# Optimization experiments

Measured on AMD Instinct MI355X. Metric: run time of the kernel, lower is better.

The kernel has to match this reference:

```python
import jax, jax.numpy as jnp
import numpy as np

N, NS, CIN, COUT, S = 65536, 16, 64, 64, 8
MID = COUT  # mid_planes = out_planes // 1
EPS = 1e-5


def _bn(t, g, b):
    # BatchNorm1d in training mode: normalize per channel over (points, neighbors)
    m = jnp.mean(t, axis=(0, 1), keepdims=True)
    v = jnp.var(t, axis=(0, 1), keepdims=True)
    return (t - m) * jax.lax.rsqrt(v + EPS) * g + b


def setup_inputs() -> dict:
    key = jax.random.key(0)
    ks = jax.random.split(key, 16)

    def w(k, shape, fan_in):
        return (jax.random.normal(k, shape, jnp.float32) / np.sqrt(fan_in)).astype(jnp.float32)

    return {
        "p": jax.random.uniform(ks[0], (N, 3), jnp.float32),
        "x": jax.random.normal(ks[1], (N, CIN), jnp.float32),
        "idx": jax.random.randint(ks[2], (N, NS), 0, N, jnp.int32),
        # q/k/v linears
        "Wq": w(ks[3], (CIN, MID), CIN), "bq": jnp.zeros((MID,), jnp.float32),
        "Wk": w(ks[4], (CIN, MID), CIN), "bk": jnp.zeros((MID,), jnp.float32),
        "Wv": w(ks[5], (CIN, COUT), CIN), "bv": jnp.zeros((COUT,), jnp.float32),
        # linear_p: Linear(3,3) -> BN(3) -> ReLU -> Linear(3,out)
        "Wp1": w(ks[6], (3, 3), 3), "bp1": jnp.zeros((3,), jnp.float32),
        "gp": jnp.ones((3,), jnp.float32), "bp_bn": jnp.zeros((3,), jnp.float32),
        "Wp2": w(ks[7], (3, COUT), 3), "bp2": jnp.zeros((COUT,), jnp.float32),
        # linear_w: BN(mid)->ReLU->Linear(mid,mid//s)->BN->ReLU->Linear(mid//s,mid//s)
        "gw1": jnp.ones((MID,), jnp.float32), "bw1_bn": jnp.zeros((MID,), jnp.float32),
        "Ww1": w(ks[8], (MID, MID // S), MID), "bw1": jnp.zeros((MID // S,), jnp.float32),
        "gw2": jnp.ones((MID // S,), jnp.float32), "bw2_bn": jnp.zeros((MID // S,), jnp.float32),
        "Ww2": w(ks[9], (MID // S, MID // S), MID // S), "bw2": jnp.zeros((MID // S,), jnp.float32),
    }


def reference(p, x, idx, Wq, bq, Wk, bk, Wv, bv, Wp1, bp1, gp, bp_bn, Wp2, bp2,
              gw1, bw1_bn, Ww1, bw1, gw2, bw2_bn, Ww2, bw2):
    # per-point projections
    xq = x @ Wq + bq                       # [N, MID]
    xk = x @ Wk + bk                       # [N, MID]
    xv = x @ Wv + bv                       # [N, COUT]
    # queryandgroup: gather neighbor features + relative xyz
    rel_p = p[idx] - p[:, None, :]         # [N, NS, 3]
    xk_g = xk[idx]                         # [N, NS, MID]
    xv_g = xv[idx]                         # [N, NS, COUT]
    # linear_p MLP on relative positions
    pr = rel_p @ Wp1 + bp1
    pr = jax.nn.relu(_bn(pr, gp, bp_bn))
    pr = pr @ Wp2 + bp2                    # [N, NS, COUT]
    # subtractive attention logits (out//mid == 1, so p_r sum is identity)
    w = xk_g - xq[:, None, :] + pr         # [N, NS, MID]
    # linear_w MLP
    w = jax.nn.relu(_bn(w, gw1, bw1_bn))
    w = w @ Ww1 + bw1                      # [N, NS, MID//S]
    w = jax.nn.relu(_bn(w, gw2, bw2_bn))
    w = w @ Ww2 + bw2                      # [N, NS, COUT//S]
    w = jax.nn.softmax(w, axis=1)          # softmax over neighbors
    # grouped weighted aggregation with shared attention planes
    n, ns, c = xv_g.shape
    out = ((xv_g + pr).reshape(n, ns, S, c // S) * w[:, :, None, :]).sum(1)
    return out.reshape(n, c)
```

## Files before the change

kernel.cpp:

```cpp
#include <hip/hip_runtime.h>

typedef unsigned short u16;
typedef __attribute__((ext_vector_type(8))) short bf16x8;
typedef __attribute__((ext_vector_type(8))) unsigned short u16x8;
typedef __attribute__((ext_vector_type(4))) float f32x4;

#define NPTS 65536
#define MTOT 1048576
#define M2TOT 131072
#define EPSb 1e-5f

#define XQ_OFF  0u
#define T_OFF   4194304u
#define ST_OFF  15728640u
#define XK_US   31457792u
#define XV_US   35652096u
#define WTQ_US  14680064u
#define WT1_US  14692352u

__device__ __forceinline__ float bf2f(u16 h) {
    return __uint_as_float(((unsigned)h) << 16);
}
__device__ __forceinline__ u16 f2bf(float f) {
    unsigned u = __float_as_uint(f);
    u += 0x7fffu + ((u >> 16) & 1u);
    return (u16)(u >> 16);
}
__device__ __forceinline__ u16 f2bf_fast(float f) {
    return (u16)((__float_as_uint(f) + 0x8000u) >> 16);
}

__global__ __launch_bounds__(256) void k0_prep(
    const float* __restrict__ Wq, const float* __restrict__ Wk,
    const float* __restrict__ Wv, const float* __restrict__ Ww1,
    float* __restrict__ ws)
{
    u16* wsu = (u16*)ws;
    const int gid = blockIdx.x * 256 + threadIdx.x;
    if (gid < 12288) {
        const float* W = (gid < 4096) ? Wq : ((gid < 8192) ? Wk : Wv);
        const int rem = gid & 4095;
        const int n = rem >> 6, c = rem & 63;
        wsu[WTQ_US + (unsigned)gid] = f2bf(W[c * 64 + n]);
    } else if (gid < 12800) {
        const int rem = gid - 12288;
        const int c = rem >> 6, r = rem & 63;
        wsu[WT1_US + (unsigned)rem] = f2bf(Ww1[r * 8 + c]);
    }
}

__global__ __launch_bounds__(256) void k1_proj_bn1(
    const float* __restrict__ p, const float* __restrict__ x, const int* __restrict__ idx,
    const float* __restrict__ bq, const float* __restrict__ bk, const float* __restrict__ bv,
    const float* __restrict__ Wp1, const float* __restrict__ bp1,
    float* __restrict__ ws)
{
    u16* wsu = (u16*)ws;
    __shared__ float sred[6];
    const int tid   = threadIdx.x;
    const int lane  = tid & 63;
    const int wid   = tid >> 6;
    const int col16 = lane & 15;
    const int quad  = lane >> 4;
    if (tid < 6) sred[tid] = 0.0f;
    __syncthreads();

    bf16x8 bf[3][4][2];
#pragma unroll
    for (int M = 0; M < 3; ++M)
#pragma unroll
        for (int t = 0; t < 4; ++t)
#pragma unroll
            for (int h = 0; h < 2; ++h)
                bf[M][t][h] = *(const bf16x8*)&wsu[WTQ_US +
                    (unsigned)(M * 4096 + (t * 16 + col16) * 64 + h * 32 + quad * 8)];

    float bq_t[4], bk_t[4], bv_t[4];
#pragma unroll
    for (int t = 0; t < 4; ++t) {
        bq_t[t] = bq[t * 16 + col16];
        bk_t[t] = bk[t * 16 + col16];
        bv_t[t] = bv[t * 16 + col16];
    }

    float* xq   = ws + XQ_OFF;
    u16*  xkb   = wsu + XK_US;
    u16*  xvb   = wsu + XV_US;

    const int gw = blockIdx.x * 4 + wid;
#pragma unroll
    for (int g = 0; g < 2; ++g) {
        const int n0 = (gw * 2 + g) * 16;
        const float* xrow = x + (unsigned)(n0 + col16) * 64u;
        const float4 fa0 = *(const float4*)&xrow[quad * 8];
        const float4 fa1 = *(const float4*)&xrow[quad * 8 + 4];
        const float4 fb0 = *(const float4*)&xrow[32 + quad * 8];
        const float4 fb1 = *(const float4*)&xrow[32 + quad * 8 + 4];
        bf16x8 a0, a1;
        a0[0] = (short)f2bf_fast(fa0.x); a0[1] = (short)f2bf_fast(fa0.y);
        a0[2] = (short)f2bf_fast(fa0.z); a0[3] = (short)f2bf_fast(fa0.w);
        a0[4] = (short)f2bf_fast(fa1.x); a0[5] = (short)f2bf_fast(fa1.y);
        a0[6] = (short)f2bf_fast(fa1.z); a0[7] = (short)f2bf_fast(fa1.w);
        a1[0] = (short)f2bf_fast(fb0.x); a1[1] = (short)f2bf_fast(fb0.y);
        a1[2] = (short)f2bf_fast(fb0.z); a1[3] = (short)f2bf_fast(fb0.w);
        a1[4] = (short)f2bf_fast(fb1.x); a1[5] = (short)f2bf_fast(fb1.y);
        a1[6] = (short)f2bf_fast(fb1.z); a1[7] = (short)f2bf_fast(fb1.w);

#pragma unroll
        for (int t = 0; t < 4; ++t) {
            f32x4 aq = {0,0,0,0}, ak = {0,0,0,0}, av = {0,0,0,0};
            aq = __builtin_amdgcn_mfma_f32_16x16x32_bf16(a0, bf[0][t][0], aq, 0, 0, 0);
            aq = __builtin_amdgcn_mfma_f32_16x16x32_bf16(a1, bf[0][t][1], aq, 0, 0, 0);
            ak = __builtin_amdgcn_mfma_f32_16x16x32_bf16(a0, bf[1][t][0], ak, 0, 0, 0);
            ak = __builtin_amdgcn_mfma_f32_16x16x32_bf16(a1, bf[1][t][1], ak, 0, 0, 0);
            av = __builtin_amdgcn_mfma_f32_16x16x32_bf16(a0, bf[2][t][0], av, 0, 0, 0);
            av = __builtin_amdgcn_mfma_f32_16x16x32_bf16(a1, bf[2][t][1], av, 0, 0, 0);
#pragma unroll
            for (int r = 0; r < 4; ++r) {
                const unsigned row = (unsigned)(n0 + quad * 4 + r);
                const unsigned o   = row * 64u + (unsigned)(t * 16 + col16);
                xq[o]  = aq[r] + bq_t[t];
                xkb[o] = f2bf(ak[r] + bk_t[t]);
                xvb[o] = f2bf(av[r] + bv_t[t]);
            }
        }
    }

    const int base = blockIdx.x * 128;
    const float w00 = Wp1[0], w01 = Wp1[1], w02 = Wp1[2];
    const float w10 = Wp1[3], w11 = Wp1[4], w12 = Wp1[5];
    const float w20 = Wp1[6], w21 = Wp1[7], w22 = Wp1[8];
    const float c0 = bp1[0], c1 = bp1[1], c2 = bp1[2];
    float s0 = 0, s1 = 0, s2 = 0, q0 = 0, q1 = 0, q2 = 0;
#pragma unroll
    for (int m = 0; m < 8; ++m) {
        const int pl = tid + m * 256;
        const int n  = base + (pl >> 4);
        const unsigned gpair = (unsigned)(base * 16 + pl);
        const int nb = idx[gpair];
        const float r0 = p[nb * 3 + 0] - p[n * 3 + 0];
        const float r1 = p[nb * 3 + 1] - p[n * 3 + 1];
        const float r2 = p[nb * 3 + 2] - p[n * 3 + 2];
        const float t0 = c0 + r0 * w00 + r1 * w10 + r2 * w20;
        const float t1 = c1 + r0 * w01 + r1 * w11 + r2 * w21;
        const float t2 = c2 + r0 * w02 + r1 * w12 + r2 * w22;
        ws[T_OFF + gpair * 3u + 0u] = t0;
        ws[T_OFF + gpair * 3u + 1u] = t1;
        ws[T_OFF + gpair * 3u + 2u] = t2;
        s0 += t0; s1 += t1; s2 += t2;
        q0 += t0 * t0; q1 += t1 * t1; q2 += t2 * t2;
    }
    atomicAdd(&sred[0], s0); atomicAdd(&sred[1], s1); atomicAdd(&sred[2], s2);
    atomicAdd(&sred[3], q0); atomicAdd(&sred[4], q1); atomicAdd(&sred[5], q2);
    __syncthreads();
    if (tid < 6) atomicAdd(&ws[ST_OFF + tid], sred[tid]);
}

__global__ __launch_bounds__(256) void k1b_bn1apply(
    const float* __restrict__ gp, const float* __restrict__ bp_bn,
    float* __restrict__ ws)
{
    const float invM = 1.0f / (float)MTOT;
    float A1[3], B1[3];
#pragma unroll
    for (int a = 0; a < 3; ++a) {
        const float mean = ws[ST_OFF + a] * invM;
        const float var  = ws[ST_OFF + 3 + a] * invM - mean * mean;
        const float sc = gp[a] * rsqrtf(var + EPSb);
        A1[a] = sc; B1[a] = bp_bn[a] - mean * sc;
    }
    const unsigned t = blockIdx.x * 256u + threadIdx.x;
    float4* Tp = (float4*)(ws + T_OFF + t * 12u);
    float4 v0 = Tp[0], v1 = Tp[1], v2 = Tp[2];
    v0.x = fmaxf(fmaf(v0.x, A1[0], B1[0]), 0.0f);
    v0.y = fmaxf(fmaf(v0.y, A1[1], B1[1]), 0.0f);
    v0.z = fmaxf(fmaf(v0.z, A1[2], B1[2]), 0.0f);
    v0.w = fmaxf(fmaf(v0.w, A1[0], B1[0]), 0.0f);
    v1.x = fmaxf(fmaf(v1.x, A1[1], B1[1]), 0.0f);
    v1.y = fmaxf(fmaf(v1.y, A1[2], B1[2]), 0.0f);
    v1.z = fmaxf(fmaf(v1.z, A1[0], B1[0]), 0.0f);
    v1.w = fmaxf(fmaf(v1.w, A1[1], B1[1]), 0.0f);
    v2.x = fmaxf(fmaf(v2.x, A1[2], B1[2]), 0.0f);
    v2.y = fmaxf(fmaf(v2.y, A1[0], B1[0]), 0.0f);
    v2.z = fmaxf(fmaf(v2.z, A1[1], B1[1]), 0.0f);
    v2.w = fmaxf(fmaf(v2.w, A1[2], B1[2]), 0.0f);
    Tp[0] = v0; Tp[1] = v1; Tp[2] = v2;
}

__global__ __launch_bounds__(256) void k2_bn2(
    const int* __restrict__ idx,
    const float* __restrict__ Wp2, const float* __restrict__ bp2,
    float* __restrict__ ws)
{
    u16* wsu = (u16*)ws;
    __shared__ float ss[64], sq[64];
    const int tid = threadIdx.x;
    const int lane = tid & 63;
    const int gw = blockIdx.x * 4 + (tid >> 6);
    if (tid < 64) { ss[tid] = 0.0f; sq[tid] = 0.0f; }

    const float wp20 = Wp2[lane], wp21 = Wp2[64 + lane], wp22 = Wp2[128 + lane];
    const float bp2c = bp2[lane];
    const float* xq  = ws + XQ_OFF;
    const float* T   = ws + T_OFF;
    const u16*  xkb  = wsu + XK_US;

    float s = 0.0f, q = 0.0f;

    for (int nn = 0; nn < 4; ++nn) {
        const int nu = __builtin_amdgcn_readfirstlane((gw * 4 + nn) * 8);

        const int4* ir4 = (const int4*)(idx + (unsigned)nu * 16u);
        const int4 i0 = ir4[0], i1 = ir4[1], i2 = ir4[2], i3 = ir4[3];
        const int nbs[16] = { i0.x, i0.y, i0.z, i0.w, i1.x, i1.y, i1.z, i1.w,
                              i2.x, i2.y, i2.z, i2.w, i3.x, i3.y, i3.z, i3.w };
        u16 kr[16];
#pragma unroll
        for (int j = 0; j < 16; ++j) kr[j] = xkb[(unsigned)nbs[j] * 64u + lane];

        float tr[48];
        const float4* Tr4 = (const float4*)(T + (unsigned)nu * 48u);
#pragma unroll
        for (int c = 0; c < 12; ++c) {
            const float4 v = Tr4[c];
            tr[4 * c + 0] = v.x; tr[4 * c + 1] = v.y;
            tr[4 * c + 2] = v.z; tr[4 * c + 3] = v.w;
        }
        const float xqc  = xq[(unsigned)nu * 64u + lane];
        const float base = bp2c - xqc;

#pragma unroll
        for (int j = 0; j < 16; ++j) {
            const float prx = base + tr[3 * j + 0] * wp20
                                   + tr[3 * j + 1] * wp21
                                   + tr[3 * j + 2] * wp22;
            const float w0 = bf2f(kr[j]) + prx;
            s += w0; q = fmaf(w0, w0, q);
        }
    }
    __syncthreads();
    atomicAdd(&ss[lane], s); atomicAdd(&sq[lane], q);
    __syncthreads();
    if (tid < 64) {
        atomicAdd(&ws[ST_OFF + 6 + tid], ss[tid]);
        atomicAdd(&ws[ST_OFF + 70 + tid], sq[tid]);
    }
}

__global__ __launch_bounds__(256) void k2b_bn3(
    const int* __restrict__ idx,
    const float* __restrict__ Wp2, const float* __restrict__ bp2,
    const float* __restrict__ gw1, const float* __restrict__ bw1_bn,
    const float* __restrict__ bw1,
    float* __restrict__ ws)
{
    u16* wsu = (u16*)ws;
    __shared__ float s3r[8], q3r[8];
    const int tid   = threadIdx.x;
    const int lane  = tid & 63;
    const int wid   = tid >> 6;
    const int col16 = lane & 15;
    const int quad  = lane >> 4;
    if (tid < 8) { s3r[tid] = 0.0f; q3r[tid] = 0.0f; }
    __syncthreads();

    const float invM2 = 1.0f / (float)M2TOT;
    float A2A[8], DA[8], WA0[8], WA1[8], WA2[8];
    float A2B[8], DB[8], WB0[8], WB1[8], WB2[8];
#pragma unroll
    for (int i = 0; i < 8; ++i) {
        {
            const int k = quad * 8 + i;
            const float mean = ws[ST_OFF + 6 + k] * invM2;
            const float var  = ws[ST_OFF + 70 + k] * invM2 - mean * mean;
            const float A2 = gw1[k] * rsqrtf(var + EPSb);
            const float B2 = bw1_bn[k] - mean * A2;
            A2A[i] = A2;
            DA[i]  = fmaf(A2, bp2[k], B2);
            WA0[i] = A2 * Wp2[k]; WA1[i] = A2 * Wp2[64 + k]; WA2[i] = A2 * Wp2[128 + k];
        }
        {
            const int k = 32 + quad * 8 + i;
            const float mean = ws[ST_OFF + 6 + k] * invM2;
            const float var  = ws[ST_OFF + 70 + k] * invM2 - mean * mean;
            const float A2 = gw1[k] * rsqrtf(var + EPSb);
            const float B2 = bw1_bn[k] - mean * A2;
            A2B[i] = A2;
            DB[i]  = fmaf(A2, bp2[k], B2);
            WB0[i] = A2 * Wp2[k]; WB1[i] = A2 * Wp2[64 + k]; WB2[i] = A2 * Wp2[128 + k];
        }
    }
    bf16x8 b0 = {0,0,0,0,0,0,0,0}, b1 = {0,0,0,0,0,0,0,0};
    if (col16 < 8) {
        b0 = *(const bf16x8*)&wsu[WT1_US + (unsigned)(col16 * 64 + quad * 8)];
        b1 = *(const bf16x8*)&wsu[WT1_US + (unsigned)(col16 * 64 + 32 + quad * 8)];
    }
    const float bw1c = (col16 < 8) ? bw1[col16] : 0.0f;

    const float* xq  = ws + XQ_OFF;
    const float* T   = ws + T_OFF;
    const u16*  xkb  = wsu + XK_US;
    const int sg = (blockIdx.x * 4 + wid) * 8;
    float bs = 0.0f, bq2 = 0.0f;

    for (int it = 0; it < 8; ++it) {
        const int nu = __builtin_amdgcn_readfirstlane((sg + it) * 8);

        const int nbv = idx[(unsigned)nu * 16u + (unsigned)col16];
        const u16* grow = xkb + (unsigned)nbv * 64u;
        const u16x8 gA = *(const u16x8*)(grow + quad * 8);
        const u16x8 gB = *(const u16x8*)(grow + 32 + quad * 8);

        const float* Trow = T + (unsigned)nu * 48u + (unsigned)col16 * 3u;
        float t0 = Trow[0];
        float t1 = Trow[1];
        float t2 = Trow[2];

        const float* xr = xq + (unsigned)nu * 64u;
        const float4 x0 = *(const float4*)(xr + quad * 8);
        const float4 x1 = *(const float4*)(xr + quad * 8 + 4);
        const float4 x2 = *(const float4*)(xr + 32 + quad * 8);
        const float4 x3 = *(const float4*)(xr + 32 + quad * 8 + 4);
        const float xqA[8] = { x0.x, x0.y, x0.z, x0.w, x1.x, x1.y, x1.z, x1.w };
        const float xqB[8] = { x2.x, x2.y, x2.z, x2.w, x3.x, x3.y, x3.z, x3.w };

        bf16x8 a0, a1;
#pragma unroll
        for (int i = 0; i < 8; ++i) {
            float vA = fmaf(-A2A[i], xqA[i], DA[i]);
            vA = fmaf(t0, WA0[i], vA);
            vA = fmaf(t1, WA1[i], vA);
            vA = fmaf(t2, WA2[i], vA);
            vA = fmaf(A2A[i], bf2f(gA[i]), vA);
            a0[i] = (short)f2bf_fast(fmaxf(vA, 0.0f));

            float vB = fmaf(-A2B[i], xqB[i], DB[i]);
            vB = fmaf(t0, WB0[i], vB);
            vB = fmaf(t1, WB1[i], vB);
            vB = fmaf(t2, WB2[i], vB);
            vB = fmaf(A2B[i], bf2f(gB[i]), vB);
            a1[i] = (short)f2bf_fast(fmaxf(vB, 0.0f));
        }
        f32x4 acc = {0.0f, 0.0f, 0.0f, 0.0f};
        acc = __builtin_amdgcn_mfma_f32_16x16x32_bf16(a0, b0, acc, 0, 0, 0);
        acc = __builtin_amdgcn_mfma_f32_16x16x32_bf16(a1, b1, acc, 0, 0, 0);
        if (col16 < 8) {
#pragma unroll
            for (int r = 0; r < 4; ++r) {
                const float o = acc[r] + bw1c;
                bs += o;
                bq2 = fmaf(o, o, bq2);
            }
        }
    }
    if (col16 < 8) {
        atomicAdd(&s3r[col16], bs);
        atomicAdd(&q3r[col16], bq2);
    }
    __syncthreads();
    if (tid < 8) {
        atomicAdd(&ws[ST_OFF + 134 + tid], s3r[tid]);
        atomicAdd(&ws[ST_OFF + 142 + tid], q3r[tid]);
    }
}

__global__ __launch_bounds__(256) void k34_fused(
    const int* __restrict__ idx,
    const float* __restrict__ Wp2, const float* __restrict__ bp2,
    const float* __restrict__ gw1, const float* __restrict__ bw1_bn,
    const float* __restrict__ bw1,
    const float* __restrict__ gw2, const float* __restrict__ bw2_bn,
    const float* __restrict__ Ww2, const float* __restrict__ bw2,
    const float* __restrict__ ws, float* __restrict__ out)
{
    const u16* wsu = (const u16*)ws;
    __shared__ float sv3[4][16][8];
    __shared__ float se[4][16][8];
    const int tid   = threadIdx.x;
    const int lane  = tid & 63;
    const int wid   = tid >> 6;
    const int col16 = lane & 15;
    const int quad  = lane >> 4;
    const int tt    = lane & 7;
    const int j1    = lane >> 3;

    const float invM2 = 1.0f / (float)M2TOT;
    float A2A[8], DA[8], WA0[8], WA1[8], WA2[8];
    float A2B[8], DB[8], WB0[8], WB1[8], WB2[8];
#pragma unroll
    for (int i = 0; i < 8; ++i) {
        {
            const int k = quad * 8 + i;
            const float mean = ws[ST_OFF + 6 + k] * invM2;
            const float var  = ws[ST_OFF + 70 + k] * invM2 - mean * mean;
            const float A2 = gw1[k] * rsqrtf(var + EPSb);
            const float B2 = bw1_bn[k] - mean * A2;
            A2A[i] = A2;
            DA[i]  = fmaf(A2, bp2[k], B2);
            WA0[i] = A2 * Wp2[k]; WA1[i] = A2 * Wp2[64 + k]; WA2[i] = A2 * Wp2[128 + k];
        }
        {
            const int k = 32 + quad * 8 + i;
            const float mean = ws[ST_OFF + 6 + k] * invM2;
            const float var  = ws[ST_OFF + 70 + k] * invM2 - mean * mean;
            const float A2 = gw1[k] * rsqrtf(var + EPSb);
            const float B2 = bw1_bn[k] - mean * A2;
            A2B[i] = A2;
            DB[i]  = fmaf(A2, bp2[k], B2);
            WB0[i] = A2 * Wp2[k]; WB1[i] = A2 * Wp2[64 + k]; WB2[i] = A2 * Wp2[128 + k];
        }
    }
    bf16x8 b0 = {0,0,0,0,0,0,0,0}, b1 = {0,0,0,0,0,0,0,0};
    if (col16 < 8) {
        b0 = *(const bf16x8*)&wsu[WT1_US + (unsigned)(col16 * 64 + quad * 8)];
        b1 = *(const bf16x8*)&wsu[WT1_US + (unsigned)(col16 * 64 + 32 + quad * 8)];
    }
    const float bw1c = (col16 < 8) ? bw1[col16] : 0.0f;
    const int   c3    = col16 & 7;
    const float mean3 = ws[ST_OFF + 134 + c3] * invM2;
    const float var3  = ws[ST_OFF + 142 + c3] * invM2 - mean3 * mean3;
    const float A3c   = gw2[c3] * rsqrtf(var3 + EPSb);
    const float B3f   = fmaf(A3c, bw1c, bw2_bn[c3] - mean3 * A3c);
    float ww2c[8];
#pragma unroll
    for (int u = 0; u < 8; ++u) ww2c[u] = Ww2[u * 8 + tt];
    const float bw2c = bw2[tt];
    const float wp20 = Wp2[lane], wp21 = Wp2[64 + lane], wp22 = Wp2[128 + lane];
    const float bp2c = bp2[lane];

    const float* xq  = ws + XQ_OFF;
    const float* T   = ws + T_OFF;
    const u16*  xkb  = wsu + XK_US;
    const u16*  xvb  = wsu + XV_US;

    const int n0 = (blockIdx.x * 4 + wid) * 16;
    for (int it = 0; it < 16; ++it) {
        const int nu = __builtin_amdgcn_readfirstlane(n0 + it);

        const int4* ir4 = (const int4*)(idx + (unsigned)nu * 16u);
        const int4 i0 = ir4[0], i1 = ir4[1], i2 = ir4[2], i3 = ir4[3];
        const int nbs[16] = { i0.x, i0.y, i0.z, i0.w, i1.x, i1.y, i1.z, i1.w,
                              i2.x, i2.y, i2.z, i2.w, i3.x, i3.y, i3.z, i3.w };
        const int nbv = idx[(unsigned)nu * 16u + (unsigned)col16];
        const u16* grow = xkb + (unsigned)nbv * 64u;
        const u16x8 gA = *(const u16x8*)(grow + quad * 8);
        const u16x8 gB = *(const u16x8*)(grow + 32 + quad * 8);
        u16 xvr[16];
#pragma unroll
        for (int j = 0; j < 16; ++j) xvr[j] = xvb[(unsigned)nbs[j] * 64u + lane];

        const float* Trow = T + (unsigned)nu * 48u + (unsigned)col16 * 3u;
        const float t0 = Trow[0];
        const float t1 = Trow[1];
        const float t2 = Trow[2];
        float tr[48];
        const float4* Tr4 = (const float4*)(T + (unsigned)nu * 48u);
#pragma unroll
        for (int c = 0; c < 12; ++c) {
            const float4 v = Tr4[c];
            tr[4 * c + 0] = v.x; tr[4 * c + 1] = v.y;
            tr[4 * c + 2] = v.z; tr[4 * c + 3] = v.w;
        }
        const float* xr = xq + (unsigned)nu * 64u;
        const float4 x0 = *(const float4*)(xr + quad * 8);
        const float4 x1 = *(const float4*)(xr + quad * 8 + 4);
        const float4 x2 = *(const float4*)(xr + 32 + quad * 8);
        const float4 x3 = *(const float4*)(xr + 32 + quad * 8 + 4);
        const float xqA[8] = { x0.x, x0.y, x0.z, x0.w, x1.x, x1.y, x1.z, x1.w };
        const float xqB[8] = { x2.x, x2.y, x2.z, x2.w, x3.x, x3.y, x3.z, x3.w };

        bf16x8 a0, a1;
#pragma unroll
        for (int i = 0; i < 8; ++i) {
            float vA = fmaf(-A2A[i], xqA[i], DA[i]);
            vA = fmaf(t0, WA0[i], vA);
            vA = fmaf(t1, WA1[i], vA);
            vA = fmaf(t2, WA2[i], vA);
            vA = fmaf(A2A[i], bf2f(gA[i]), vA);
            a0[i] = (short)f2bf_fast(fmaxf(vA, 0.0f));

            float vB = fmaf(-A2B[i], xqB[i], DB[i]);
            vB = fmaf(t0, WB0[i], vB);
            vB = fmaf(t1, WB1[i], vB);
            vB = fmaf(t2, WB2[i], vB);
            vB = fmaf(A2B[i], bf2f(gB[i]), vB);
            a1[i] = (short)f2bf_fast(fmaxf(vB, 0.0f));
        }
        f32x4 acc = {0.0f, 0.0f, 0.0f, 0.0f};
        acc = __builtin_amdgcn_mfma_f32_16x16x32_bf16(a0, b0, acc, 0, 0, 0);
        acc = __builtin_amdgcn_mfma_f32_16x16x32_bf16(a1, b1, acc, 0, 0, 0);

        if (col16 < 8) {
#pragma unroll
            for (int r = 0; r < 4; ++r)
                sv3[wid][quad * 4 + r][col16] = fmaxf(fmaf(A3c, acc[r], B3f), 0.0f);
        }
        float s0 = bw2c, s1 = bw2c;
#pragma unroll
        for (int u = 0; u < 8; ++u) {
            s0 = fmaf(sv3[wid][j1][u], ww2c[u], s0);
            s1 = fmaf(sv3[wid][j1 + 8][u], ww2c[u], s1);
        }
        float mx = fmaxf(s0, s1);
        mx = fmaxf(mx, __shfl_xor(mx, 8));
        mx = fmaxf(mx, __shfl_xor(mx, 16));
        mx = fmaxf(mx, __shfl_xor(mx, 32));
        const float e0 = __expf(s0 - mx);
        const float e1 = __expf(s1 - mx);
        float sm = e0 + e1;
        sm += __shfl_xor(sm, 8);
        sm += __shfl_xor(sm, 16);
        sm += __shfl_xor(sm, 32);
        const float rs = __builtin_amdgcn_rcpf(sm);
        se[wid][j1][tt]     = e0 * rs;
        se[wid][j1 + 8][tt] = e1 * rs;

        float xvacc = 0.0f, ta0 = 0.0f, ta1 = 0.0f, ta2 = 0.0f;
#pragma unroll
        for (int j = 0; j < 16; ++j) {
            const float ej = se[wid][j][tt];
            xvacc = fmaf(bf2f(xvr[j]), ej, xvacc);
            ta0 = fmaf(tr[3 * j + 0], ej, ta0);
            ta1 = fmaf(tr[3 * j + 1], ej, ta1);
            ta2 = fmaf(tr[3 * j + 2], ej, ta2);
        }
        out[(unsigned)nu * 64u + lane] =
            fmaf(ta0, wp20, fmaf(ta1, wp21, fmaf(ta2, wp22, xvacc + bp2c)));
    }
}

extern "C" void kernel_launch(void* const* d_in, const int* in_sizes, int n_in,
                              void* d_out, int out_size, void* d_ws, size_t ws_size,
                              hipStream_t stream)
{
    const float* p      = (const float*)d_in[0];
    const float* x      = (const float*)d_in[1];
    const int*   idx    = (const int*)d_in[2];
    const float* Wq     = (const float*)d_in[3];
    const float* bq     = (const float*)d_in[4];
    const float* Wk     = (const float*)d_in[5];
    const float* bk     = (const float*)d_in[6];
    const float* Wv     = (const float*)d_in[7];
    const float* bv     = (const float*)d_in[8];
    const float* Wp1    = (const float*)d_in[9];
    const float* bp1    = (const float*)d_in[10];
    const float* gp     = (const float*)d_in[11];
    const float* bp_bn  = (const float*)d_in[12];
    const float* Wp2    = (const float*)d_in[13];
    const float* bp2    = (const float*)d_in[14];
    const float* gw1    = (const float*)d_in[15];
    const float* bw1_bn = (const float*)d_in[16];
    const float* Ww1    = (const float*)d_in[17];
    const float* bw1    = (const float*)d_in[18];
    const float* gw2    = (const float*)d_in[19];
    const float* bw2_bn = (const float*)d_in[20];
    const float* Ww2    = (const float*)d_in[21];
    const float* bw2    = (const float*)d_in[22];
    float* ws  = (float*)d_ws;
    float* out = (float*)d_out;
    (void)in_sizes; (void)n_in; (void)out_size; (void)ws_size;

    hipMemsetAsync((char*)d_ws + (size_t)ST_OFF * 4, 0, 150 * sizeof(float), stream);

    k0_prep<<<50, 256, 0, stream>>>(Wq, Wk, Wv, Ww1, ws);
    k1_proj_bn1<<<512, 256, 0, stream>>>(p, x, idx, bq, bk, bv, Wp1, bp1, ws);
    k1b_bn1apply<<<1024, 256, 0, stream>>>(gp, bp_bn, ws);
    k2_bn2<<<512, 256, 0, stream>>>(idx, Wp2, bp2, ws);
    k2b_bn3<<<256, 256, 0, stream>>>(idx, Wp2, bp2, gw1, bw1_bn, bw1, ws);
    k34_fused<<<1024, 256, 0, stream>>>(idx, Wp2, bp2, gw1, bw1_bn, bw1,
                                        gw2, bw2_bn, Ww2, bw2, ws, out);
}
```

Before: 256.1 us.

## Drop weight-prep kernel, use packed bf16 conversion and f32x2 math, double k34 grid

Measured after the change: 271.3 us. 1.06x slower.

```diff
diff --git a/kernel.cpp b/kernel.cpp
--- a/kernel.cpp
+++ b/kernel.cpp
@@ -2,7 +2,7 @@
 
 typedef unsigned short u16;
 typedef __attribute__((ext_vector_type(8))) short bf16x8;
-typedef __attribute__((ext_vector_type(8))) unsigned short u16x8;
+typedef __attribute__((ext_vector_type(2))) float f32x2;
 typedef __attribute__((ext_vector_type(4))) float f32x4;
 
 #define NPTS 65536
@@ -15,8 +15,6 @@
 #define ST_OFF  15728640u
 #define XK_US   31457792u
 #define XV_US   35652096u
-#define WTQ_US  14680064u
-#define WT1_US  14692352u
 
 __device__ __forceinline__ float bf2f(u16 h) {
     return __uint_as_float(((unsigned)h) << 16);
@@ -26,36 +24,94 @@
     u += 0x7fffu + ((u >> 16) & 1u);
     return (u16)(u >> 16);
 }
-__device__ __forceinline__ u16 f2bf_fast(float f) {
-    return (u16)((__float_as_uint(f) + 0x8000u) >> 16);
-}
-
-__global__ __launch_bounds__(256) void k0_prep(
-    const float* __restrict__ Wq, const float* __restrict__ Wk,
-    const float* __restrict__ Wv, const float* __restrict__ Ww1,
-    float* __restrict__ ws)
-{
-    u16* wsu = (u16*)ws;
-    const int gid = blockIdx.x * 256 + threadIdx.x;
-    if (gid < 12288) {
-        const float* W = (gid < 4096) ? Wq : ((gid < 8192) ? Wk : Wv);
-        const int rem = gid & 4095;
-        const int n = rem >> 6, c = rem & 63;
-        wsu[WTQ_US + (unsigned)gid] = f2bf(W[c * 64 + n]);
-    } else if (gid < 12800) {
-        const int rem = gid - 12288;
-        const int c = rem >> 6, r = rem & 63;
-        wsu[WT1_US + (unsigned)rem] = f2bf(Ww1[r * 8 + c]);
+__device__ __forceinline__ unsigned cvt_pk_bf16(float lo, float hi) {
+    unsigned r;
+    asm("v_cvt_pk_bf16_f32 %0, %1, %2" : "=v"(r) : "v"(lo), "v"(hi));
+    return r;
+}
+__device__ __forceinline__ bf16x8 pack_bf8(const float4 lo, const float4 hi) {
+    union { bf16x8 v; unsigned u[4]; } r;
+    r.u[0] = cvt_pk_bf16(lo.x, lo.y);
+    r.u[1] = cvt_pk_bf16(lo.z, lo.w);
+    r.u[2] = cvt_pk_bf16(hi.x, hi.y);
+    r.u[3] = cvt_pk_bf16(hi.z, hi.w);
+    return r.v;
+}
+
+struct BN2C {
+    f32x2 A2[4], D[4], W0[4], W1[4], W2[4];
+};
+__device__ __forceinline__ void bn2c_build(
+    BN2C& c, const int kbase, const float* __restrict__ ws,
+    const float* __restrict__ gw1, const float* __restrict__ bw1_bn,
+    const float* __restrict__ bp2, const float* __restrict__ Wp2)
+{
+    const float invM2 = 1.0f / (float)M2TOT;
+#pragma unroll
+    for (int j = 0; j < 4; ++j) {
+        float a2[2], d[2], w0[2], w1[2], w2[2];
+#pragma unroll
+        for (int h = 0; h < 2; ++h) {
+            const int k = kbase + 2 * j + h;
+            const float mean = ws[ST_OFF + 6 + k] * invM2;
+            const float var  = ws[ST_OFF + 70 + k] * invM2 - mean * mean;
+            const float A2 = gw1[k] * rsqrtf(var + EPSb);
+            const float B2 = bw1_bn[k] - mean * A2;
+            a2[h] = A2; d[h] = fmaf(A2, bp2[k], B2);
+            w0[h] = A2 * Wp2[k]; w1[h] = A2 * Wp2[64 + k]; w2[h] = A2 * Wp2[128 + k];
+        }
+        c.A2[j] = f32x2{a2[0], a2[1]}; c.D[j] = f32x2{d[0], d[1]};
+        c.W0[j] = f32x2{w0[0], w0[1]}; c.W1[j] = f32x2{w1[0], w1[1]};
+        c.W2[j] = f32x2{w2[0], w2[1]};
+    }
+}
+__device__ __forceinline__ bf16x8 build_frag(
+    const BN2C& c, const f32x2 t0v, const f32x2 t1v, const f32x2 t2v,
+    const uint4 g, const float4 xlo, const float4 xhi)
+{
+    union { bf16x8 v; unsigned u[4]; } r;
+    const unsigned gu[4] = { g.x, g.y, g.z, g.w };
+    const f32x2 xp[4] = { {xlo.x, xlo.y}, {xlo.z, xlo.w}, {xhi.x, xhi.y}, {xhi.z, xhi.w} };
+#pragma unroll
+    for (int j = 0; j < 4; ++j) {
+        f32x2 gf;
+        gf.x = __uint_as_float(gu[j] << 16);
+        gf.y = __uint_as_float(gu[j] & 0xffff0000u);
+        f32x2 v = c.D[j] - c.A2[j] * xp[j];
+        v = v + t0v * c.W0[j];
+        v = v + t1v * c.W1[j];
+        v = v + t2v * c.W2[j];
+        v = v + c.A2[j] * gf;
+        r.u[j] = cvt_pk_bf16(fmaxf(v.x, 0.0f), fmaxf(v.y, 0.0f));
+    }
+    return r.v;
+}
+
+__device__ __forceinline__ void load_b_frags(
+    const float* __restrict__ Ww1, const int col16, const int quad,
+    bf16x8& b0, bf16x8& b1)
+{
+    b0 = bf16x8{0,0,0,0,0,0,0,0};
+    b1 = bf16x8{0,0,0,0,0,0,0,0};
+    if (col16 < 8) {
+#pragma unroll
+        for (int j = 0; j < 8; ++j) {
+            const int k0 = quad * 8 + j;
+            b0[j] = (short)f2bf(Ww1[k0 * 8 + col16]);
+            b1[j] = (short)f2bf(Ww1[(k0 + 32) * 8 + col16]);
+        }
     }
 }
 
 __global__ __launch_bounds__(256) void k1_proj_bn1(
     const float* __restrict__ p, const float* __restrict__ x, const int* __restrict__ idx,
+    const float* __restrict__ Wq, const float* __restrict__ Wk, const float* __restrict__ Wv,
     const float* __restrict__ bq, const float* __restrict__ bk, const float* __restrict__ bv,
     const float* __restrict__ Wp1, const float* __restrict__ bp1,
     float* __restrict__ ws)
 {
     u16* wsu = (u16*)ws;
+    __shared__ u16 wtab[12288];
     __shared__ float sred[6];
     const int tid   = threadIdx.x;
     const int lane  = tid & 63;
@@ -63,6 +119,15 @@
     const int col16 = lane & 15;
     const int quad  = lane >> 4;
     if (tid < 6) sred[tid] = 0.0f;
+
+#pragma unroll
+    for (int k = 0; k < 48; ++k) {
+        const int e = tid + k * 256;
+        const float* W = (e < 4096) ? Wq : ((e < 8192) ? Wk : Wv);
+        const int rem = e & 4095;
+        const int n = rem >> 6, c = rem & 63;
+        wtab[e] = f2bf(W[c * 64 + n]);
+    }
     __syncthreads();
 
     bf16x8 bf[3][4][2];
@@ -72,7 +137,7 @@
         for (int t = 0; t < 4; ++t)
 #pragma unroll
             for (int h = 0; h < 2; ++h)
-                bf[M][t][h] = *(const bf16x8*)&wsu[WTQ_US +
+                bf[M][t][h] = *(const bf16x8*)&wtab[
                     (unsigned)(M * 4096 + (t * 16 + col16) * 64 + h * 32 + quad * 8)];
 
     float bq_t[4], bk_t[4], bv_t[4];
@@ -96,15 +161,8 @@
         const float4 fa1 = *(const float4*)&xrow[quad * 8 + 4];
         const float4 fb0 = *(const float4*)&xrow[32 + quad * 8];
         const float4 fb1 = *(const float4*)&xrow[32 + quad * 8 + 4];
-        bf16x8 a0, a1;
-        a0[0] = (short)f2bf_fast(fa0.x); a0[1] = (short)f2bf_fast(fa0.y);
-        a0[2] = (short)f2bf_fast(fa0.z); a0[3] = (short)f2bf_fast(fa0.w);
-        a0[4] = (short)f2bf_fast(fa1.x); a0[5] = (short)f2bf_fast(fa1.y);
-        a0[6] = (short)f2bf_fast(fa1.z); a0[7] = (short)f2bf_fast(fa1.w);
-        a1[0] = (short)f2bf_fast(fb0.x); a1[1] = (short)f2bf_fast(fb0.y);
-        a1[2] = (short)f2bf_fast(fb0.z); a1[3] = (short)f2bf_fast(fb0.w);
-        a1[4] = (short)f2bf_fast(fb1.x); a1[5] = (short)f2bf_fast(fb1.y);
-        a1[6] = (short)f2bf_fast(fb1.z); a1[7] = (short)f2bf_fast(fb1.w);
+        const bf16x8 a0 = pack_bf8(fa0, fa1);
+        const bf16x8 a1 = pack_bf8(fb0, fb1);
 
 #pragma unroll
         for (int t = 0; t < 4; ++t) {
@@ -251,7 +309,7 @@
     const int* __restrict__ idx,
     const float* __restrict__ Wp2, const float* __restrict__ bp2,
     const float* __restrict__ gw1, const float* __restrict__ bw1_bn,
-    const float* __restrict__ bw1,
+    const float* __restrict__ Ww1, const float* __restrict__ bw1,
     float* __restrict__ ws)
 {
     u16* wsu = (u16*)ws;
@@ -264,37 +322,12 @@
     if (tid < 8) { s3r[tid] = 0.0f; q3r[tid] = 0.0f; }
     __syncthreads();
 
-    const float invM2 = 1.0f / (float)M2TOT;
-    float A2A[8], DA[8], WA0[8], WA1[8], WA2[8];
-    float A2B[8], DB[8], WB0[8], WB1[8], WB2[8];
-#pragma unroll
-    for (int i = 0; i < 8; ++i) {
-        {
-            const int k = quad * 8 + i;
-            const float mean = ws[ST_OFF + 6 + k] * invM2;
-            const float var  = ws[ST_OFF + 70 + k] * invM2 - mean * mean;
-            const float A2 = gw1[k] * rsqrtf(var + EPSb);
-            const float B2 = bw1_bn[k] - mean * A2;
-            A2A[i] = A2;
-            DA[i]  = fmaf(A2, bp2[k], B2);
-            WA0[i] = A2 * Wp2[k]; WA1[i] = A2 * Wp2[64 + k]; WA2[i] = A2 * Wp2[128 + k];
-        }
-        {
-            const int k = 32 + quad * 8 + i;
-            const float mean = ws[ST_OFF + 6 + k] * invM2;
-            const float var  = ws[ST_OFF + 70 + k] * invM2 - mean * mean;
-            const float A2 = gw1[k] * rsqrtf(var + EPSb);
-            const float B2 = bw1_bn[k] - mean * A2;
-            A2B[i] = A2;
-            DB[i]  = fmaf(A2, bp2[k], B2);
-            WB0[i] = A2 * Wp2[k]; WB1[i] = A2 * Wp2[64 + k]; WB2[i] = A2 * Wp2[128 + k];
-        }
-    }
-    bf16x8 b0 = {0,0,0,0,0,0,0,0}, b1 = {0,0,0,0,0,0,0,0};
-    if (col16 < 8) {
-        b0 = *(const bf16x8*)&wsu[WT1_US + (unsigned)(col16 * 64 + quad * 8)];
-        b1 = *(const bf16x8*)&wsu[WT1_US + (unsigned)(col16 * 64 + 32 + quad * 8)];
-    }
+    BN2C cA, cB;
+    bn2c_build(cA, quad * 8,      ws, gw1, bw1_bn, bp2, Wp2);
+    bn2c_build(cB, 32 + quad * 8, ws, gw1, bw1_bn, bp2, Wp2);
+
+    bf16x8 b0, b1;
+    load_b_frags(Ww1, col16, quad, b0, b1);
     const float bw1c = (col16 < 8) ? bw1[col16] : 0.0f;
 
     const float* xq  = ws + XQ_OFF;
@@ -308,39 +341,23 @@
 
         const int nbv = idx[(unsigned)nu * 16u + (unsigned)col16];
         const u16* grow = xkb + (unsigned)nbv * 64u;
-        const u16x8 gA = *(const u16x8*)(grow + quad * 8);
-        const u16x8 gB = *(const u16x8*)(grow + 32 + quad * 8);
+        const uint4 gA = *(const uint4*)(grow + quad * 8);
+        const uint4 gB = *(const uint4*)(grow + 32 + quad * 8);
 
         const float* Trow = T + (unsigned)nu * 48u + (unsigned)col16 * 3u;
-        float t0 = Trow[0];
-        float t1 = Trow[1];
-        float t2 = Trow[2];
+        const f32x2 t0v = f32x2{Trow[0], Trow[0]};
+        const f32x2 t1v = f32x2{Trow[1], Trow[1]};
+        const f32x2 t2v = f32x2{Trow[2], Trow[2]};
 
         const float* xr = xq + (unsigned)nu * 64u;
         const float4 x0 = *(const float4*)(xr + quad * 8);
         const float4 x1 = *(const float4*)(xr + quad * 8 + 4);
         const float4 x2 = *(const float4*)(xr + 32 + quad * 8);
         const float4 x3 = *(const float4*)(xr + 32 + quad * 8 + 4);
-        const float xqA[8] = { x0.x, x0.y, x0.z, x0.w, x1.x, x1.y, x1.z, x1.w };
-        const float xqB[8] = { x2.x, x2.y, x2.z, x2.w, x3.x, x3.y, x3.z, x3.w };
-
-        bf16x8 a0, a1;
-#pragma unroll
-        for (int i = 0; i < 8; ++i) {
-            float vA = fmaf(-A2A[i], xqA[i], DA[i]);
-            vA = fmaf(t0, WA0[i], vA);
-            vA = fmaf(t1, WA1[i], vA);
-            vA = fmaf(t2, WA2[i], vA);
-            vA = fmaf(A2A[i], bf2f(gA[i]), vA);
-            a0[i] = (short)f2bf_fast(fmaxf(vA, 0.0f));
-
-            float vB = fmaf(-A2B[i], xqB[i], DB[i]);
-            vB = fmaf(t0, WB0[i], vB);
-            vB = fmaf(t1, WB1[i], vB);
-            vB = fmaf(t2, WB2[i], vB);
-            vB = fmaf(A2B[i], bf2f(gB[i]), vB);
-            a1[i] = (short)f2bf_fast(fmaxf(vB, 0.0f));
-        }
+
+        const bf16x8 a0 = build_frag(cA, t0v, t1v, t2v, gA, x0, x1);
+        const bf16x8 a1 = build_frag(cB, t0v, t1v, t2v, gB, x2, x3);
+
         f32x4 acc = {0.0f, 0.0f, 0.0f, 0.0f};
         acc = __builtin_amdgcn_mfma_f32_16x16x32_bf16(a0, b0, acc, 0, 0, 0);
         acc = __builtin_amdgcn_mfma_f32_16x16x32_bf16(a1, b1, acc, 0, 0, 0);
@@ -368,7 +385,7 @@
     const int* __restrict__ idx,
     const float* __restrict__ Wp2, const float* __restrict__ bp2,
     const float* __restrict__ gw1, const float* __restrict__ bw1_bn,
-    const float* __restrict__ bw1,
+    const float* __restrict__ Ww1, const float* __restrict__ bw1,
     const float* __restrict__ gw2, const float* __restrict__ bw2_bn,
     const float* __restrict__ Ww2, const float* __restrict__ bw2,
     const float* __restrict__ ws, float* __restrict__ out)
@@ -385,36 +402,12 @@
     const int j1    = lane >> 3;
 
     const float invM2 = 1.0f / (float)M2TOT;
-    float A2A[8], DA[8], WA0[8], WA1[8], WA2[8];
-    float A2B[8], DB[8], WB0[8], WB1[8], WB2[8];
-#pragma unroll
-    for (int i = 0; i < 8; ++i) {
-        {
-            const int k = quad * 8 + i;
-            const float mean = ws[ST_OFF + 6 + k] * invM2;
-            const float var  = ws[ST_OFF + 70 + k] * invM2 - mean * mean;
-            const float A2 = gw1[k] * rsqrtf(var + EPSb);
-            const float B2 = bw1_bn[k] - mean * A2;
-            A2A[i] = A2;
-            DA[i]  = fmaf(A2, bp2[k], B2);
-            WA0[i] = A2 * Wp2[k]; WA1[i] = A2 * Wp2[64 + k]; WA2[i] = A2 * Wp2[128 + k];
-        }
-        {
-            const int k = 32 + quad * 8 + i;
-            const float mean = ws[ST_OFF + 6 + k] * invM2;
-            const float var  = ws[ST_OFF + 70 + k] * invM2 - mean * mean;
-            const float A2 = gw1[k] * rsqrtf(var + EPSb);
-            const float B2 = bw1_bn[k] - mean * A2;
-            A2B[i] = A2;
-            DB[i]  = fmaf(A2, bp2[k], B2);
-            WB0[i] = A2 * Wp2[k]; WB1[i] = A2 * Wp2[64 + k]; WB2[i] = A2 * Wp2[128 + k];
-        }
-    }
-    bf16x8 b0 = {0,0,0,0,0,0,0,0}, b1 = {0,0,0,0,0,0,0,0};
-    if (col16 < 8) {
-        b0 = *(const bf16x8*)&wsu[WT1_US + (unsigned)(col16 * 64 + quad * 8)];
-        b1 = *(const bf16x8*)&wsu[WT1_US + (unsigned)(col16 * 64 + 32 + quad * 8)];
-    }
+    BN2C cA, cB;
+    bn2c_build(cA, quad * 8,      ws, gw1, bw1_bn, bp2, Wp2);
+    bn2c_build(cB, 32 + quad * 8, ws, gw1, bw1_bn, bp2, Wp2);
+
+    bf16x8 b0, b1;
+    load_b_frags(Ww1, col16, quad, b0, b1);
     const float bw1c = (col16 < 8) ? bw1[col16] : 0.0f;
     const int   c3    = col16 & 7;
     const float mean3 = ws[ST_OFF + 134 + c3] * invM2;
@@ -433,8 +426,8 @@
     const u16*  xkb  = wsu + XK_US;
     const u16*  xvb  = wsu + XV_US;
 
-    const int n0 = (blockIdx.x * 4 + wid) * 16;
-    for (int it = 0; it < 16; ++it) {
+    const int n0 = (blockIdx.x * 4 + wid) * 8;
+    for (int it = 0; it < 8; ++it) {
         const int nu = __builtin_amdgcn_readfirstlane(n0 + it);
 
         const int4* ir4 = (const int4*)(idx + (unsigned)nu * 16u);
@@ -443,16 +436,16 @@
                               i2.x, i2.y, i2.z, i2.w, i3.x, i3.y, i3.z, i3.w };
         const int nbv = idx[(unsigned)nu * 16u + (unsigned)col16];
         const u16* grow = xkb + (unsigned)nbv * 64u;
-        const u16x8 gA = *(const u16x8*)(grow + quad * 8);
-        const u16x8 gB = *(const u16x8*)(grow + 32 + quad * 8);
+        const uint4 gA = *(const uint4*)(grow + quad * 8);
+        const uint4 gB = *(const uint4*)(grow + 32 + quad * 8);
         u16 xvr[16];
 #pragma unroll
         for (int j = 0; j < 16; ++j) xvr[j] = xvb[(unsigned)nbs[j] * 64u + lane];
 
         const float* Trow = T + (unsigned)nu * 48u + (unsigned)col16 * 3u;
-        const float t0 = Trow[0];
-        const float t1 = Trow[1];
-        const float t2 = Trow[2];
+        const f32x2 t0v = f32x2{Trow[0], Trow[0]};
+        const f32x2 t1v = f32x2{Trow[1], Trow[1]};
+        const f32x2 t2v = f32x2{Trow[2], Trow[2]};
         float tr[48];
         const float4* Tr4 = (const float4*)(T + (unsigned)nu * 48u);
 #pragma unroll
@@ -466,26 +459,10 @@
         const float4 x1 = *(const float4*)(xr + quad * 8 + 4);
         const float4 x2 = *(const float4*)(xr + 32 + quad * 8);
         const float4 x3 = *(const float4*)(xr + 32 + quad * 8 + 4);
-        const float xqA[8] = { x0.x, x0.y, x0.z, x0.w, x1.x, x1.y, x1.z, x1.w };
-        const float xqB[8] = { x2.x, x2.y, x2.z, x2.w, x3.x, x3.y, x3.z, x3.w };
-
-        bf16x8 a0, a1;
-#pragma unroll
-        for (int i = 0; i < 8; ++i) {
-            float vA = fmaf(-A2A[i], xqA[i], DA[i]);
-            vA = fmaf(t0, WA0[i], vA);
-            vA = fmaf(t1, WA1[i], vA);
-            vA = fmaf(t2, WA2[i], vA);
-            vA = fmaf(A2A[i], bf2f(gA[i]), vA);
-            a0[i] = (short)f2bf_fast(fmaxf(vA, 0.0f));
-
-            float vB = fmaf(-A2B[i], xqB[i], DB[i]);
-            vB = fmaf(t0, WB0[i], vB);
-            vB = fmaf(t1, WB1[i], vB);
-            vB = fmaf(t2, WB2[i], vB);
-            vB = fmaf(A2B[i], bf2f(gB[i]), vB);
-            a1[i] = (short)f2bf_fast(fmaxf(vB, 0.0f));
-        }
+
+        const bf16x8 a0 = build_frag(cA, t0v, t1v, t2v, gA, x0, x1);
+        const bf16x8 a1 = build_frag(cB, t0v, t1v, t2v, gB, x2, x3);
+
         f32x4 acc = {0.0f, 0.0f, 0.0f, 0.0f};
         acc = __builtin_amdgcn_mfma_f32_16x16x32_bf16(a0, b0, acc, 0, 0, 0);
         acc = __builtin_amdgcn_mfma_f32_16x16x32_bf16(a1, b1, acc, 0, 0, 0);
@@ -562,11 +539,11 @@
 
     hipMemsetAsync((char*)d_ws + (size_t)ST_OFF * 4, 0, 150 * sizeof(float), stream);
 
-    k0_prep<<<50, 256, 0, stream>>>(Wq, Wk, Wv, Ww1, ws);
-    k1_proj_bn1<<<512, 256, 0, stream>>>(p, x, idx, bq, bk, bv, Wp1, bp1, ws);
+    k1_proj_bn1<<<512, 256, 0, stream>>>(p, x, idx, Wq, Wk, Wv,
+                                         bq, bk, bv, Wp1, bp1, ws);
     k1b_bn1apply<<<1024, 256, 0, stream>>>(gp, bp_bn, ws);
     k2_bn2<<<512, 256, 0, stream>>>(idx, Wp2, bp2, ws);
-    k2b_bn3<<<256, 256, 0, stream>>>(idx, Wp2, bp2, gw1, bw1_bn, bw1, ws);
-    k34_fused<<<1024, 256, 0, stream>>>(idx, Wp2, bp2, gw1, bw1_bn, bw1,
+    k2b_bn3<<<256, 256, 0, stream>>>(idx, Wp2, bp2, gw1, bw1_bn, Ww1, bw1, ws);
+    k34_fused<<<2048, 256, 0, stream>>>(idx, Wp2, bp2, gw1, bw1_bn, Ww1, bw1,
                                         gw2, bw2_bn, Ww2, bw2, ws, out);
 }
```
